# Kernel optimization log

Hardware: AMD Instinct MI355X
Metric: run time of the kernel (lower is better)

## Reference

```python
import jax, jax.numpy as jnp
import numpy as np

# Module dims (match init_kwargs / input_specs)
V = 25        # number of graph nodes (chain skeleton)
K = 3         # max receptive-field size (neighbors incl. self), padded
CIN = 64
COUT = 64
N = 16
T = 512
TK = 3        # temporal_kernel
PAD = TK // 2 # time_pad default


def _build_graph():
    # Chain adjacency with self-links: node i <-> {i-1, i, i+1}
    A = np.zeros((V, V), np.float32)
    for i in range(V):
        A[i, i] = 1.0
        if i > 0:
            A[i, i - 1] = 1.0
        if i < V - 1:
            A[i, i + 1] = 1.0
    # Pad each node's neighbor list to K entries; mask marks real neighbors.
    idx = np.zeros((V, K), np.int32)
    mask = np.zeros((V, K), bool)
    for i in range(V):
        nb = np.where(A[i] != 0)[0]
        idx[i, : len(nb)] = nb
        mask[i, : len(nb)] = True
    return idx, mask


def setup_inputs() -> dict:
    key = jax.random.key(0)
    k_x, k_w, k_b = jax.random.split(key, 3)
    x = jax.random.normal(k_x, (N, CIN, V, T), dtype=jnp.float32)
    # One Conv2d kernel per node: [V, C_out, C_in, K, TK]; padded neighbor
    # slots are zeroed via mask inside reference().
    W = jax.random.normal(k_w, (V, COUT, CIN, K, TK), dtype=jnp.float32) * 0.05
    b = jax.random.normal(k_b, (V, COUT), dtype=jnp.float32) * 0.05
    idx_np, mask_np = _build_graph()
    return {
        "x": x,
        "W": W,
        "b": b,
        "idx": jnp.asarray(idx_np),
        "mask": jnp.asarray(mask_np),
    }


def reference(x, W, b, idx, mask):
    # x: [N, C, V, T]; W: [V, O, C, K, TK]; b: [V, O]; idx/mask: [V, K]
    Tt = x.shape[-1]
    # Zero out padded neighbor slots so padded rows contribute nothing
    # (equivalent to torch's variable-height per-node kernels).
    Wm = jnp.where(mask[:, None, None, :, None], W, 0.0)
    # Temporal zero padding (Conv2d padding=(0, time_pad))
    xp = jnp.pad(x, ((0, 0), (0, 0), (0, 0), (PAD, PAD)))
    # Batched neighbor gather: [N, C, V, K, T + 2*PAD]
    g = xp[:, :, idx, :]
    # Cross-correlation over the TK temporal taps (stride 1)
    out = jnp.zeros((x.shape[0], W.shape[1], V, Tt), dtype=x.dtype)
    for kt in range(TK):
        out = out + jnp.einsum(
            "ncvkt,vock->novt", g[..., kt : kt + Tt], Wm[..., kt]
        )
    out = out + b.T[None, :, :, None]  # per-node bias [O, V]
    return out
```

## Files before the change

### kernel.cpp

```cpp
#include <hip/hip_runtime.h>
#include <hip/hip_bf16.h>

#define NB   16
#define CINC 64
#define COUTC 64
#define NV   25
#define TLEN 512
#define KK   3
#define TKK  3

typedef short short8 __attribute__((ext_vector_type(8)));
typedef float f32x4  __attribute__((ext_vector_type(4)));
typedef float f32x16 __attribute__((ext_vector_type(16)));

#define XT_ROWS 514
#define XS_BYTES 16640
#define NWT3BLK (NV * 9)

__device__ __forceinline__ unsigned pack_bf16(float lo, float hi) {
  __hip_bfloat16 l = __float2bfloat16(lo);
  __hip_bfloat16 h = __float2bfloat16(hi);
  unsigned short ul = *reinterpret_cast<unsigned short*>(&l);
  unsigned short uh = *reinterpret_cast<unsigned short*>(&h);
  return (unsigned)ul | ((unsigned)uh << 16);
}

__global__ __launch_bounds__(256) void prep_all(
    const float* __restrict__ x, const float* __restrict__ W,
    const unsigned char* __restrict__ mask_raw,
    __hip_bfloat16* __restrict__ Wt3, __hip_bfloat16* __restrict__ xT) {
  __shared__ float ts[64][65];
  int bid = blockIdx.x;
  if (bid < NWT3BLK) {
    int blk = bid;
    int v = blk / 9, kkt = blk % 9, k = kkt / 3, kt = kkt % 3;
    const int* mi = (const int*)mask_raw;
    int ok = 1;
    for (int i = 0; i < 18; ++i) {
      int m = mi[i];
      if (m != 0 && m != 1) ok = 0;
    }
    int m = ok ? mi[v * KK + k] : (int)(mask_raw[v * KK + k] != 0);
    const float* Wv = W + (size_t)v * COUTC * CINC * 9;
    __hip_bfloat16* dst = Wt3 + (size_t)blk * 4096;
    for (int i = threadIdx.x; i < 4096; i += 256) {
      int e     = i & 7;
      int lane  = (i >> 3) & 63;
      int ks    = (i >> 9) & 3;
      int oslab = i >> 11;
      int o = oslab * 32 + (lane & 31);
      int c = ks * 16 + 8 * (lane >> 5) + e;
      float val = m ? Wv[(o * CINC + c) * 9 + k * 3 + kt] : 0.f;
      dst[i] = __float2bfloat16(val);
    }
    return;
  }
  bid -= NWT3BLK;
  const int tb = (bid & 7) * 64;
  const int vn = bid >> 3;
  const int v  = vn % NV;
  const int n  = vn / NV;
  const int tid = threadIdx.x;
  for (int i = tid; i < 1024; i += 256) {
    int c = i >> 4, tq = (i & 15) * 4;
    float4 val = *(const float4*)(x + (((size_t)n * CINC + c) * NV + v) * TLEN + tb + tq);
    ts[c][tq + 0] = val.x;
    ts[c][tq + 1] = val.y;
    ts[c][tq + 2] = val.z;
    ts[c][tq + 3] = val.w;
  }
  __syncthreads();
  unsigned* base = (unsigned*)(xT + ((size_t)(n * NV + v) * XT_ROWS) * CINC);
  for (int i = tid; i < 2048; i += 256) {
    int c2 = i & 31, t = i >> 5;
    base[(tb + 1 + t) * 32 + c2] = pack_bf16(ts[2 * c2][t], ts[2 * c2 + 1][t]);
  }
  if (tb == 0 && tid < 32) base[tid] = 0u;
  if (tb == TLEN - 64 && tid < 32) base[513 * 32 + tid] = 0u;
}

__device__ __forceinline__ const char* slab_base(const __hip_bfloat16* xT,
                                                 int n, int vk, int tb) {
  return (const char*)xT + ((size_t)(n * NV + vk) * XT_ROWS + tb) * 128;
}

__global__ __launch_bounds__(256, 3) void lcn_mfma32(
    const __hip_bfloat16* __restrict__ xT,
    const __hip_bfloat16* __restrict__ Wt3,
    const float* __restrict__ bias,
    const int* __restrict__ idx,
    float* __restrict__ out) {
  __shared__ char xs[KK][XS_BYTES];

  const int tb   = blockIdx.x * 128;
  const int n    = blockIdx.y;
  const int v    = blockIdx.z;
  const int tid  = threadIdx.x;
  const int lane = tid & 63;
  const int wave = tid >> 6;
  const int os   = wave & 1;
  const int th   = wave >> 1;
  const int hi   = lane >> 5;
  const int l31  = lane & 31;

  {
    const char* g0 = slab_base(xT, n, idx[v * KK + 0], tb);
    const char* g1 = slab_base(xT, n, idx[v * KK + 1], tb);
    const char* g2 = slab_base(xT, n, idx[v * KK + 2], tb);
    for (int j = wave; j < 3 * 17; j += 4) {
      int slab = j / 17, c = j % 17;
      const char* gb = slab == 0 ? g0 : (slab == 1 ? g1 : g2);
      int L = c * 1024 + lane * 16;
      if (L < XS_BYTES) {
        int g = L ^ (((L >> 7) & 7) << 4);
        __builtin_amdgcn_global_load_lds(
            (const __attribute__((address_space(1))) void*)(gb + g),
            (__attribute__((address_space(3))) void*)(&xs[slab][c * 1024]),
            16, 0, 0);
      }
    }
  }
  __syncthreads();

  f32x16 acc0 = {}, acc1 = {};

#pragma unroll 1
  for (int k = 0; k < KK; ++k) {
    const char* cb = xs[k];
    short8 a[TKK][4];
    {
      const short8* wb = (const short8*)Wt3 +
                         ((size_t)((v * KK + k) * TKK) * 2 + os) * 256 + lane;
#pragma unroll
      for (int kt = 0; kt < TKK; ++kt)
#pragma unroll
        for (int ks = 0; ks < 4; ++ks)
          a[kt][ks] = wb[kt * 512 + (ks << 6)];
    }
#pragma unroll
    for (int kt = 0; kt < TKK; ++kt) {
      {
        const int r  = th * 64 + l31 + kt;
        const int sw = (r & 7) << 4;
        const int co = hi * 16;
        const char* bp = cb + r * 128;
#pragma unroll
        for (int ks = 0; ks < 4; ++ks) {
          short8 bfr = *(const short8*)(bp + ((co + 32 * ks) ^ sw));
          acc0 = __builtin_amdgcn_mfma_f32_32x32x16_bf16(a[kt][ks], bfr, acc0, 0, 0, 0);
        }
      }
      {
        const int r  = th * 64 + 32 + l31 + kt;
        const int sw = (r & 7) << 4;
        const int co = hi * 16;
        const char* bp = cb + r * 128;
#pragma unroll
        for (int ks = 0; ks < 4; ++ks) {
          short8 bfr = *(const short8*)(bp + ((co + 32 * ks) ^ sw));
          acc1 = __builtin_amdgcn_mfma_f32_32x32x16_bf16(a[kt][ks], bfr, acc1, 0, 0, 0);
        }
      }
    }
  }

  const float* bv = bias + v * COUTC;
#pragma unroll
  for (int s = 0; s < 2; ++s) {
    const f32x16& acc = s ? acc1 : acc0;
    const int t = tb + th * 64 + s * 32 + l31;
#pragma unroll
    for (int reg = 0; reg < 16; ++reg) {
      int o = os * 32 + 4 * hi + (reg & 3) + 8 * (reg >> 2);
      out[(((size_t)n * COUTC + o) * NV + v) * TLEN + t] = acc[reg] + bv[o];
    }
  }
}

__global__ void prep_mask_kernel(const int* __restrict__ mask_raw,
                                 int* __restrict__ mask_out) {
  __shared__ int fmt;
  if (threadIdx.x == 0) {
    int ok = 1;
    for (int i = 0; i < 18; ++i) {
      int m = mask_raw[i];
      if (m != 0 && m != 1) ok = 0;
    }
    fmt = ok;
  }
  __syncthreads();
  int i = threadIdx.x;
  if (i < NV * KK) {
    int m;
    if (fmt) m = mask_raw[i];
    else     m = (((const unsigned char*)mask_raw)[i] != 0) ? 1 : 0;
    mask_out[i] = m;
  }
}

__global__ void prep_wt_kernel(const float* __restrict__ W,
                               float* __restrict__ Wt) {
  int v   = blockIdx.x / 9;
  int kkt = blockIdx.x % 9;
  const float* Wv = W + (size_t)v * COUTC * CINC * 9;
  float* dst = Wt + (size_t)blockIdx.x * (CINC * COUTC);
  for (int i = threadIdx.x; i < CINC * COUTC; i += 256) {
    int c = i >> 6;
    int o = i & 63;
    dst[i] = Wv[(o * CINC + c) * 9 + kkt];
  }
}

__global__ __launch_bounds__(256, 4) void lcn_main(
    const float* __restrict__ x, const float* __restrict__ Wt,
    const float* __restrict__ b, const int* __restrict__ idx,
    const int* __restrict__ maskn, float* __restrict__ out) {
  __shared__ float xsf[CINC][66];
  __shared__ float wsh[CINC][COUTC];
  const int tb  = blockIdx.x * 64;
  const int v   = blockIdx.y;
  const int n   = blockIdx.z;
  const int tid = threadIdx.x;
  const int t0  = tid & 63;
  const int og  = tid >> 6;
  float acc[16];
#pragma unroll
  for (int j = 0; j < 16; ++j) acc[j] = 0.f;
  for (int k = 0; k < KK; ++k) {
    const int vk = idx[v * KK + k];
    const int mk = maskn[v * KK + k];
    __syncthreads();
    for (int i = tid; i < CINC * 66; i += 256) {
      int c  = i / 66;
      int tt = i - c * 66;
      int gt = tb - 1 + tt;
      float val = 0.f;
      if (mk && gt >= 0 && gt < TLEN)
        val = x[(((size_t)n * CINC + c) * NV + vk) * TLEN + gt];
      xsf[c][tt] = val;
    }
    for (int kt = 0; kt < TKK; ++kt) {
      __syncthreads();
      const float4* src =
          (const float4*)(Wt + ((size_t)(v * KK + k) * TKK + kt) * (CINC * COUTC));
      for (int i = tid; i < CINC * COUTC / 4; i += 256)
        ((float4*)wsh)[i] = src[i];
      __syncthreads();
#pragma unroll 4
      for (int c = 0; c < CINC; ++c) {
        float xv = xsf[c][t0 + kt];
        const float4* wrow = (const float4*)&wsh[c][og * 16];
#pragma unroll
        for (int j4 = 0; j4 < 4; ++j4) {
          float4 wv = wrow[j4];
          acc[j4 * 4 + 0] = fmaf(wv.x, xv, acc[j4 * 4 + 0]);
          acc[j4 * 4 + 1] = fmaf(wv.y, xv, acc[j4 * 4 + 1]);
          acc[j4 * 4 + 2] = fmaf(wv.z, xv, acc[j4 * 4 + 2]);
          acc[j4 * 4 + 3] = fmaf(wv.w, xv, acc[j4 * 4 + 3]);
        }
      }
    }
  }
#pragma unroll
  for (int j = 0; j < 16; ++j) {
    int o = og * 16 + j;
    out[(((size_t)n * COUTC + o) * NV + v) * TLEN + tb + t0] =
        acc[j] + b[v * COUTC + o];
  }
}

extern "C" void kernel_launch(void* const* d_in, const int* in_sizes, int n_in,
                              void* d_out, int out_size, void* d_ws, size_t ws_size,
                              hipStream_t stream) {
  const float* x    = (const float*)d_in[0];
  const float* W    = (const float*)d_in[1];
  const float* b    = (const float*)d_in[2];
  const int*   idx  = (const int*)d_in[3];
  const void*  mask = (const void*)d_in[4];
  float* out = (float*)d_out;

  const size_t WT3_BYTES = (size_t)NV * 9 * 4096 * sizeof(__hip_bfloat16);
  const size_t XT_BYTES  = (size_t)NB * NV * XT_ROWS * CINC * sizeof(__hip_bfloat16);
  const size_t NEED      = 512 + WT3_BYTES + XT_BYTES + 2048;

  if (ws_size >= NEED) {
    __hip_bfloat16* Wt3 = (__hip_bfloat16*)((char*)d_ws + 512);
    __hip_bfloat16* xT  = (__hip_bfloat16*)((char*)d_ws + 512 + WT3_BYTES);
    hipLaunchKernelGGL(prep_all, dim3(NWT3BLK + 8 * NV * NB), dim3(256), 0,
                       stream, x, W, (const unsigned char*)mask, Wt3, xT);
    hipLaunchKernelGGL(lcn_mfma32, dim3(TLEN / 128, NB, NV), dim3(256), 0,
                       stream, xT, Wt3, b, idx, out);
  } else {
    int*   maskn = (int*)d_ws;
    float* Wt    = (float*)((char*)d_ws + 512);
    hipLaunchKernelGGL(prep_mask_kernel, dim3(1), dim3(128), 0, stream,
                       (const int*)mask, maskn);
    hipLaunchKernelGGL(prep_wt_kernel, dim3(NV * KK * TKK), dim3(256), 0, stream,
                       W, Wt);
    hipLaunchKernelGGL(lcn_main, dim3(TLEN / 64, NV, NB), dim3(256), 0, stream,
                       x, Wt, b, idx, maskn, out);
  }
}
```

Before: 54.31 us.

## Pipeline per-neighbor LDS slab loads with compute using partial vmcnt waits

Replaces the single full-barrier wait after loading all three neighbor slabs with staged s_waitcnt vmcnt counts, so compute on slab 0 can begin while slabs 1 and 2 are still arriving. Every wave now issues a uniform number of global-to-LDS loads per slab, with dummy loads into a scratch LDS buffer, so the vmcnt thresholds hold. Weight fragments for the next neighbor are prefetched into registers before computing the current one. This aims to hide global load latency, at the cost of more LDS, more registers and fragile hand-tuned wait counts.

New measurement: 46.65 us. 1.16x faster.

```diff
diff --git a/kernel.cpp b/kernel.cpp
--- a/kernel.cpp
+++ b/kernel.cpp
@@ -14,7 +14,7 @@
 typedef float f32x16 __attribute__((ext_vector_type(16)));
 
 #define XT_ROWS 514
-#define XS_BYTES 16640
+#define XS_STRIDE 17408
 #define NWT3BLK (NV * 9)
 
 __device__ __forceinline__ unsigned pack_bf16(float lo, float hi) {
@@ -90,7 +90,8 @@
     const float* __restrict__ bias,
     const int* __restrict__ idx,
     float* __restrict__ out) {
-  __shared__ char xs[KK][XS_BYTES];
+  __shared__ char xs[KK][XS_STRIDE];
+  __shared__ char xs_dummy[1024];
 
   const int tb   = blockIdx.x * 128;
   const int n    = blockIdx.y;
@@ -103,66 +104,99 @@
   const int hi   = lane >> 5;
   const int l31  = lane & 31;
 
+#define LOAD_A(DST, KIDX)                                                     \
+  {                                                                           \
+    const short8* wb = (const short8*)Wt3 +                                   \
+        ((size_t)((v * KK + (KIDX)) * TKK) * 2 + os) * 256 + lane;            \
+    _Pragma("unroll") for (int kt = 0; kt < TKK; ++kt)                        \
+      _Pragma("unroll") for (int ks = 0; ks < 4; ++ks)                        \
+        DST[kt * 4 + ks] = wb[kt * 512 + (ks << 6)];                          \
+  }
+
+#define COMPUTE_K(CB, A)                                                      \
+  _Pragma("unroll") for (int kt = 0; kt < TKK; ++kt) {                        \
+    {                                                                         \
+      const int r  = th * 64 + l31 + kt;                                      \
+      const int sw = (r & 7) << 4;                                            \
+      const int co = hi * 16;                                                 \
+      const char* bp = (CB) + r * 128;                                        \
+      _Pragma("unroll") for (int ks = 0; ks < 4; ++ks) {                      \
+        short8 bfr = *(const short8*)(bp + ((co + 32 * ks) ^ sw));            \
+        acc0 = __builtin_amdgcn_mfma_f32_32x32x16_bf16(A[kt * 4 + ks], bfr,   \
+                                                       acc0, 0, 0, 0);        \
+      }                                                                       \
+    }                                                                         \
+    {                                                                         \
+      const int r  = th * 64 + 32 + l31 + kt;                                 \
+      const int sw = (r & 7) << 4;                                            \
+      const int co = hi * 16;                                                 \
+      const char* bp = (CB) + r * 128;                                        \
+      _Pragma("unroll") for (int ks = 0; ks < 4; ++ks) {                      \
+        short8 bfr = *(const short8*)(bp + ((co + 32 * ks) ^ sw));            \
+        acc1 = __builtin_amdgcn_mfma_f32_32x32x16_bf16(A[kt * 4 + ks], bfr,   \
+                                                       acc1, 0, 0, 0);        \
+      }                                                                       \
+    }                                                                         \
+  }
+
+  short8 aP[12], aQ[12];
+  LOAD_A(aP, 0)
+  __builtin_amdgcn_sched_barrier(0);
   {
-    const char* g0 = slab_base(xT, n, idx[v * KK + 0], tb);
-    const char* g1 = slab_base(xT, n, idx[v * KK + 1], tb);
-    const char* g2 = slab_base(xT, n, idx[v * KK + 2], tb);
-    for (int j = wave; j < 3 * 17; j += 4) {
-      int slab = j / 17, c = j % 17;
-      const char* gb = slab == 0 ? g0 : (slab == 1 ? g1 : g2);
-      int L = c * 1024 + lane * 16;
-      if (L < XS_BYTES) {
+    const char* gb0 = slab_base(xT, n, idx[v * KK + 0], tb);
+    const char* gb1 = slab_base(xT, n, idx[v * KK + 1], tb);
+    const char* gb2 = slab_base(xT, n, idx[v * KK + 2], tb);
+#pragma unroll
+    for (int s = 0; s < KK; ++s) {
+      const char* gb = (s == 0) ? gb0 : ((s == 1) ? gb1 : gb2);
+#pragma unroll
+      for (int q = 0; q < 4; ++q) {
+        int c = wave + q * 4;
+        int L = c * 1024 + lane * 16;
         int g = L ^ (((L >> 7) & 7) << 4);
         __builtin_amdgcn_global_load_lds(
             (const __attribute__((address_space(1))) void*)(gb + g),
-            (__attribute__((address_space(3))) void*)(&xs[slab][c * 1024]),
+            (__attribute__((address_space(3))) void*)(&xs[s][c * 1024]),
             16, 0, 0);
       }
-    }
-  }
-  __syncthreads();
+      if (wave == 0) {
+        int L = 16 * 1024 + lane * 16;
+        int g = L ^ (((L >> 7) & 7) << 4);
+        __builtin_amdgcn_global_load_lds(
+            (const __attribute__((address_space(1))) void*)(gb + g),
+            (__attribute__((address_space(3))) void*)(&xs[s][16 * 1024]),
+            16, 0, 0);
+      } else {
+        __builtin_amdgcn_global_load_lds(
+            (const __attribute__((address_space(1))) void*)(gb + lane * 16),
+            (__attribute__((address_space(3))) void*)(xs_dummy),
+            16, 0, 0);
+      }
+      __builtin_amdgcn_sched_barrier(0);
+    }
+  }
 
   f32x16 acc0 = {}, acc1 = {};
 
-#pragma unroll 1
-  for (int k = 0; k < KK; ++k) {
-    const char* cb = xs[k];
-    short8 a[TKK][4];
-    {
-      const short8* wb = (const short8*)Wt3 +
-                         ((size_t)((v * KK + k) * TKK) * 2 + os) * 256 + lane;
-#pragma unroll
-      for (int kt = 0; kt < TKK; ++kt)
-#pragma unroll
-        for (int ks = 0; ks < 4; ++ks)
-          a[kt][ks] = wb[kt * 512 + (ks << 6)];
-    }
-#pragma unroll
-    for (int kt = 0; kt < TKK; ++kt) {
-      {
-        const int r  = th * 64 + l31 + kt;
-        const int sw = (r & 7) << 4;
-        const int co = hi * 16;
-        const char* bp = cb + r * 128;
-#pragma unroll
-        for (int ks = 0; ks < 4; ++ks) {
-          short8 bfr = *(const short8*)(bp + ((co + 32 * ks) ^ sw));
-          acc0 = __builtin_amdgcn_mfma_f32_32x32x16_bf16(a[kt][ks], bfr, acc0, 0, 0, 0);
-        }
-      }
-      {
-        const int r  = th * 64 + 32 + l31 + kt;
-        const int sw = (r & 7) << 4;
-        const int co = hi * 16;
-        const char* bp = cb + r * 128;
-#pragma unroll
-        for (int ks = 0; ks < 4; ++ks) {
-          short8 bfr = *(const short8*)(bp + ((co + 32 * ks) ^ sw));
-          acc1 = __builtin_amdgcn_mfma_f32_32x32x16_bf16(a[kt][ks], bfr, acc1, 0, 0, 0);
-        }
-      }
-    }
-  }
+  asm volatile("s_waitcnt vmcnt(10)" ::: "memory");
+  __builtin_amdgcn_s_barrier();
+  __builtin_amdgcn_sched_barrier(0);
+  LOAD_A(aQ, 1)
+  COMPUTE_K(xs[0], aP)
+
+  asm volatile("s_waitcnt vmcnt(17)" ::: "memory");
+  __builtin_amdgcn_s_barrier();
+  __builtin_amdgcn_sched_barrier(0);
+  COMPUTE_K(xs[1], aQ)
+
+  asm volatile("s_waitcnt vmcnt(12)" ::: "memory");
+  __builtin_amdgcn_s_barrier();
+  __builtin_amdgcn_sched_barrier(0);
+  LOAD_A(aP, 2)
+  COMPUTE_K(xs[2], aP)
+
+#undef LOAD_A
+#undef COMPUTE_K
 
   const float* bv = bias + v * COUTC;
 #pragma unroll
```
